# Kernel optimization log

Hardware: AMD Instinct MI355X
Metric: run time of the kernel (lower is better)

The kernel has to match this reference:

```python
import jax, jax.numpy as jnp
import numpy as np

P_BU = 0.5  # y_bottom_up_percent
P_TD = 1.0 - P_BU
EPS = 1e-12


def l2n(w):
    # F.normalize(w, dim=1)
    n = jnp.linalg.norm(w, axis=1, keepdims=True)
    return w / jnp.maximum(n, EPS)


def setup_inputs() -> dict:
    key = jax.random.key(0)
    ks = jax.random.split(key, 5)
    X, Y, Z = 64 * 64, 16384, 100
    return {
        "x": jax.random.normal(ks[0], (1, 64, 64), dtype=jnp.float32),
        "z": jax.random.randint(ks[1], (1,), 0, Z, dtype=jnp.int64 if jax.config.jax_enable_x64 else jnp.int32).astype(jnp.int32),
        "per_item": 10,
        "x2y_w": jax.random.uniform(ks[2], (Y, X), dtype=jnp.float32),
        "z2y_w": jax.random.uniform(ks[3], (Y, Z), dtype=jnp.float32),
        "y2z_w": jax.random.uniform(ks[4], (Z, Y), dtype=jnp.float32),
        "age_y": jnp.zeros((Y,), dtype=jnp.float32),
        "age_z": jnp.zeros((Z,), dtype=jnp.float32),
        "thr": jnp.zeros((Y,), dtype=jnp.float32),
    }


def _train_loop(xv, zh, z_idx, per_item, x2y_w, z2y_w, y2z_w, age_y, age_z, thr):
    Y = age_y.shape[0]

    def step(carry, _):
        x2y_w, z2y_w, y2z_w, age_y, age_z, thr = carry
        x2y_w = l2n(x2y_w)
        z2y_w = l2n(z2y_w)
        y2z_w = l2n(y2z_w)
        # pre-response: bottom-up + top-down, shape [Y]
        y_pre = (P_BU * (xv @ x2y_w.T) + P_TD * (zh @ z2y_w.T))[0]
        i0 = jnp.argmax(y_pre)
        r0 = y_pre[i0]
        # top_k_competition(flag=1): keep winner if above threshold or young
        keep = (r0 > thr[i0]) | (age_y[i0] < 1.0)
        unact = jnp.where(age_y >= 1.0, 0.0, 1.0)
        has_unact = jnp.sum(unact) > 0
        alt = jnp.argmax(y_pre * unact)
        win = jnp.where(keep, i0, jnp.where(has_unact, alt, i0))
        # Hebbian/EMA row updates with lr = 1/(age+1) (age before increment)
        lr = 1.0 / (age_y[win] + 1.0)
        x2y_w = x2y_w.at[win].set((1.0 - lr) * x2y_w[win] + lr * xv[0])
        z2y_w = z2y_w.at[win].set((1.0 - lr) * z2y_w[win] + lr * zh[0])
        age_y = age_y.at[win].add(1.0)
        zlr = (1.0 / (age_z[z_idx] + 1.0)) * zh[0, z_idx]
        y_onehot = jnp.zeros((Y,), x2y_w.dtype).at[win].set(1.0)
        y2z_w = y2z_w.at[z_idx].set((1.0 - zlr) * y2z_w[z_idx] + zlr * y_onehot)
        age_z = age_z.at[z_idx].add(1.0)
        thr = thr.at[win].set(lr * r0 + (1.0 - lr) * thr[win])
        return (x2y_w, z2y_w, y2z_w, age_y, age_z, thr), None

    carry, _ = jax.lax.scan(step, (x2y_w, z2y_w, y2z_w, age_y, age_z, thr), None, length=per_item)
    return carry


def reference(x, z, per_item, x2y_w, z2y_w, y2z_w, age_y, age_z, thr):
    # mode == 'train' path of DN.forward, batch = 1
    xv = x.reshape(1, -1)
    xv = xv / jnp.maximum(jnp.linalg.norm(xv, axis=1, keepdims=True), EPS)
    Z = z2y_w.shape[1]
    zh = jax.nn.one_hot(z, Z, dtype=xv.dtype)  # one-hot is already unit L2 norm
    z_idx = z[0]

    x2y_w, z2y_w, y2z_w, age_y, age_z, thr = _train_loop(
        xv, zh, z_idx, per_item, x2y_w, z2y_w, y2z_w, age_y, age_z, thr)

    x2y_w = l2n(x2y_w)
    y2z_w = l2n(y2z_w)
    y_flag = jnp.where(age_y >= 1.0, 1.0, 0.0)  # activated-neuron mask
    y_temp = (xv @ x2y_w.T) * y_flag[None, :]
    # top_k_competition(flag=0): one-hot at argmax
    y = jnp.zeros_like(y_temp).at[0, jnp.argmax(y_temp[0])].set(1.0)
    output = y @ y2z_w.T  # trans_y forward is identity on y_act
    y_activated_num = jnp.sum(y_flag)
    return output, y_activated_num
```

## Files before the change

kernel.cpp:

```cpp
#include <hip/hip_runtime.h>
#include <cmath>

#define EPSN 1e-12f
#define CHUNK 128
#define NCH 128
#define NTL 128
#define MAPCAP 16

__device__ __forceinline__ void amax_combine(float& v, int& i, float ov, int oi) {
    if (ov > v || (ov == v && oi < i)) { v = ov; i = oi; }
}
__device__ __forceinline__ void wave_amax(float& v, int& i) {
    for (int off = 32; off; off >>= 1) {
        float a = __shfl_down(v, off, 64);
        int b = __shfl_down(i, off, 64);
        amax_combine(v, i, a, b);
    }
}

__global__ __launch_bounds__(256) void k_prep(
    const float* __restrict__ x2y, const float* __restrict__ z2y,
    const float* __restrict__ y2z, const int* __restrict__ zptr,
    const float* __restrict__ x,
    float* __restrict__ dotx, float* __restrict__ nw2,
    float* __restrict__ valz, float* __restrict__ nz2,
    float* __restrict__ nry, float* __restrict__ xn2, int* __restrict__ cnti,
    int X, int Y, int Z)
{
    const int bid = blockIdx.x;
    const int NBZ = Y / 4;
    const int tid = threadIdx.x;
    const int lane = tid & 63, wv = tid >> 6;
    if (bid < NBZ) {
        const int zv = zptr[0];
        const int row = bid * 4 + wv;
        const float* r = z2y + (size_t)row * Z;
        float q = 0.f, v = 0.f;
        for (int j = lane; j < Z; j += 64) {
            float e = r[j];
            q += e * e;
            if (j == zv) v = e;
        }
        for (int off = 32; off; off >>= 1) {
            q += __shfl_down(q, off, 64);
            v += __shfl_down(v, off, 64);
        }
        if (lane == 0) { nz2[row] = q; valz[row] = v; }
    } else if (bid < NBZ + Z) {
        const int row = bid - NBZ;
        const float4* r4 = (const float4*)(y2z + (size_t)row * Y);
        float q = 0.f;
        for (int i = tid; i < (Y >> 2); i += 256) {
            float4 w = r4[i];
            q += w.x*w.x + w.y*w.y + w.z*w.z + w.w*w.w;
        }
        for (int off = 32; off; off >>= 1) q += __shfl_down(q, off, 64);
        __shared__ float sq[4];
        if (lane == 0) sq[wv] = q;
        __syncthreads();
        if (tid == 0) nry[row] = sq[0] + sq[1] + sq[2] + sq[3];
    } else if (bid < NBZ + Z + Y) {
        const int row = bid - NBZ - Z;
        const float4* w4 = (const float4*)(x2y + (size_t)row * X);
        const float4* x4 = (const float4*)x;
        float d = 0.f, q = 0.f;
        for (int i = tid; i < (X >> 2); i += 256) {
            float4 w = w4[i]; float4 xx = x4[i];
            d += w.x*xx.x + w.y*xx.y + w.z*xx.z + w.w*xx.w;
            q += w.x*w.x + w.y*w.y + w.z*w.z + w.w*w.w;
        }
        for (int off = 32; off; off >>= 1) {
            d += __shfl_down(d, off, 64);
            q += __shfl_down(q, off, 64);
        }
        __shared__ float sd[4], sq2[4];
        if (lane == 0) { sd[wv] = d; sq2[wv] = q; }
        __syncthreads();
        if (tid == 0) {
            dotx[row] = sd[0] + sd[1] + sd[2] + sd[3];
            nw2[row]  = sq2[0] + sq2[1] + sq2[2] + sq2[3];
        }
    } else {
        const float4* x4 = (const float4*)x;
        float q = 0.f;
        for (int i = tid; i < (X >> 2); i += 256) {
            float4 xx = x4[i];
            q += xx.x*xx.x + xx.y*xx.y + xx.z*xx.z + xx.w*xx.w;
        }
        for (int off = 32; off; off >>= 1) q += __shfl_down(q, off, 64);
        __shared__ float sq3[4];
        if (lane == 0) sq3[wv] = q;
        __syncthreads();
        if (tid == 0) { xn2[0] = sq3[0]+sq3[1]+sq3[2]+sq3[3]; cnti[0] = 0; }
    }
}

__global__ __launch_bounds__(NTL) void k_combine(
    const float* __restrict__ age_y_in, const float* __restrict__ thr_in,
    const float* __restrict__ y2z, const int* __restrict__ zptr,
    const float* __restrict__ dotx, const float* __restrict__ nw2,
    const float* __restrict__ valz, const float* __restrict__ nz2,
    const float* __restrict__ xn2,
    float* __restrict__ yp_ws, float* __restrict__ cA_ws,
    float* __restrict__ chv, int* __restrict__ chi,
    float* __restrict__ chcv, int* __restrict__ chci,
    float* __restrict__ cthr, float* __restrict__ cage,
    float* __restrict__ cvz, float* __restrict__ cnz,
    float* __restrict__ cyz, float* __restrict__ ccc,
    int* __restrict__ cnti, int Y)
{
    const int b = blockIdx.x, t = threadIdx.x;
    const int e = b * CHUNK + t;
    const int lane = t & 63, wv = t >> 6;
    const int zv = zptr[0];
    const float xn = fmaxf(sqrtf(xn2[0]), EPSN);
    const float vz_e = valz[e], nz_e = nz2[e];
    const float thr_e = thr_in[e];
    const float yz_e = y2z[(size_t)zv * Y + e];
    const float c = dotx[e] / (fmaxf(sqrtf(nw2[e]), EPSN) * xn);
    const float s = vz_e / fmaxf(sqrtf(nz_e), EPSN);
    const float ypv = 0.5f * (c + s);
    const float agev = age_y_in[e];
    const int young = agev < 1.0f;
    cA_ws[e] = c;
    yp_ws[e] = ypv;
    float v1 = ypv; int i1 = e;
    float v2 = c * (young ? 0.0f : 1.0f); int i2 = e;
    int yc = young;
    wave_amax(v1, i1);
    wave_amax(v2, i2);
    for (int off = 32; off; off >>= 1) yc += __shfl_down(yc, off, 64);
    __shared__ float s1v[2]; __shared__ int s1i[2];
    __shared__ float s2v[2]; __shared__ int s2i[2];
    __shared__ int syc[2]; __shared__ int sh_c1;
    if (lane == 0) { s1v[wv] = v1; s1i[wv] = i1; s2v[wv] = v2; s2i[wv] = i2; syc[wv] = yc; }
    __syncthreads();
    if (t == 0) {
        float a = s1v[0]; int ai = s1i[0];
        amax_combine(a, ai, s1v[1], s1i[1]);
        float bmv = s2v[0]; int bmi = s2i[0];
        amax_combine(bmv, bmi, s2v[1], s2i[1]);
        chv[b] = a; chi[b] = ai; chcv[b] = bmv; chci[b] = bmi;
        sh_c1 = ai;
        atomicAdd(cnti, syc[0] + syc[1]);
    }
    __syncthreads();
    if (e == sh_c1) {
        cthr[b] = thr_e; cage[b] = agev; cvz[b] = vz_e;
        cnz[b] = nz_e;   cyz[b] = yz_e;  ccc[b] = c;
    }
}

#define UPD(WIN, Gthr, Gage, Gvz, Gnz, Gy2z, Gc) do { \
    const int w_ = (WIN); \
    float age_o = (Gage), thr_o = (Gthr), c_o = (Gc); \
    float s_o = (Gvz) / fmaxf(sqrtf((Gnz)), EPSN); \
    int e_ = -1; \
    _Pragma("unroll") \
    for (int k_ = 0; k_ < MAPCAP; ++k_) if (wmI[k_] == w_) { \
        age_o = wmAge[k_]; thr_o = wmThr[k_]; s_o = wmS[k_]; c_o = wmC[k_]; e_ = k_; } \
    const float lr_ = 1.f/(age_o+1.f), om_ = 1.f-lr_; \
    const float cn_ = (om_*c_o+lr_)/fmaxf(sqrtf(om_*om_+lr_*lr_+2.f*lr_*om_*c_o), EPSN); \
    const float sn_ = (om_*s_o+lr_)/fmaxf(sqrtf(om_*om_+lr_*lr_+2.f*lr_*om_*s_o), EPSN); \
    if (e_ < 0) { e_ = wmn; wmn++; } \
    _Pragma("unroll") \
    for (int k_ = 0; k_ < MAPCAP; ++k_) if (k_ == e_) { \
        wmI[k_] = w_; wmAge[k_] = age_o + 1.f; wmThr[k_] = lr_*r0 + om_*thr_o; \
        wmS[k_] = sn_; wmC[k_] = cn_; wmYp[k_] = 0.5f*(cn_+sn_); } \
    if (age_o < 1.f && age_o + 1.f >= 1.f) cnt--; \
    { const int cw_ = (w_) >> 7; \
      if (lane == (cw_ & 63)) { \
        if (cw_ & 64) amax_combine(chc1, chcI1, cn_, w_); \
        else          amax_combine(chc0, chcI0, cn_, w_); } } \
    const float L_ = fmaxf(sqrtf(beta*beta*N0sq + 2.f*beta*Aacc + Bacc), EPSN); \
    beta /= L_; Aacc /= L_; Bacc /= (L_*L_); \
    _Pragma("unroll") \
    for (int k_ = 0; k_ < MAPCAP; ++k_) ymG[k_] /= L_; \
    const float zlr_ = 1.f/(agez+1.f), oz_ = 1.f-zlr_; \
    beta *= oz_; Aacc *= oz_; Bacc *= oz_*oz_; \
    _Pragma("unroll") \
    for (int k_ = 0; k_ < MAPCAP; ++k_) ymG[k_] *= oz_; \
    int q_ = -1; \
    _Pragma("unroll") \
    for (int k_ = 0; k_ < MAPCAP; ++k_) if (ymI[k_] == w_) q_ = k_; \
    if (q_ < 0) { q_ = ymn; ymn++; \
        _Pragma("unroll") \
        for (int k_ = 0; k_ < MAPCAP; ++k_) if (k_ == q_) { \
            ymI[k_] = w_; ymG[k_] = 0.f; ymV0[k_] = (Gy2z); } } \
    float gold_ = 0.f, v0_ = 0.f; \
    _Pragma("unroll") \
    for (int k_ = 0; k_ < MAPCAP; ++k_) if (k_ == q_) { gold_ = ymG[k_]; v0_ = ymV0[k_]; } \
    Bacc += 2.f*zlr_*gold_ + zlr_*zlr_; \
    Aacc += zlr_*v0_; \
    _Pragma("unroll") \
    for (int k_ = 0; k_ < MAPCAP; ++k_) if (k_ == q_) ymG[k_] = gold_ + zlr_; \
    agez += 1.f; \
    win = w_; \
} while (0)

__global__ __launch_bounds__(64) void k_loop(
    const int* __restrict__ zptr, const int* __restrict__ pitem,
    const float* __restrict__ y2z,
    const float* __restrict__ age_y_in, const float* __restrict__ age_z_in,
    const float* __restrict__ thr_in,
    const float* __restrict__ valz, const float* __restrict__ nz2,
    const float* __restrict__ nry,
    const float* __restrict__ yp_ws, const float* __restrict__ cA_ws,
    const float* __restrict__ chv_g, const int* __restrict__ chi_g,
    const float* __restrict__ chcv_g, const int* __restrict__ chci_g,
    const float* __restrict__ cthr, const float* __restrict__ cage,
    const float* __restrict__ cvz, const float* __restrict__ cnz,
    const float* __restrict__ cyz, const float* __restrict__ ccc,
    const int* __restrict__ cnti,
    float* __restrict__ out, int Y, int Z)
{
    const int lane = threadIdx.x;
    const int zv = zptr[0];
    const float* __restrict__ y2zrow = y2z + (size_t)zv * Y;

    float chv0 = chv_g[lane], chv1 = chv_g[lane + 64];
    int   chi0 = chi_g[lane], chi1 = chi_g[lane + 64];
    float chc0 = chcv_g[lane], chc1 = chcv_g[lane + 64];
    int   chcI0 = chci_g[lane], chcI1 = chci_g[lane + 64];
    float pthr0 = cthr[lane], pthr1 = cthr[lane + 64];
    float page0 = cage[lane], page1 = cage[lane + 64];
    float pvz0  = cvz[lane],  pvz1  = cvz[lane + 64];
    float pnz0  = cnz[lane],  pnz1  = cnz[lane + 64];
    float pyz0  = cyz[lane],  pyz1  = cyz[lane + 64];
    float pca0  = ccc[lane],  pca1  = ccc[lane + 64];

    int cnt = cnti[0];
    float N0sq = nry[zv], agez = age_z_in[zv];
    float beta = 1.f, Aacc = 0.f, Bacc = 0.f;
    int wmn = 0, ymn = 0;
    int   wmI[MAPCAP]; float wmAge[MAPCAP], wmThr[MAPCAP], wmS[MAPCAP], wmC[MAPCAP], wmYp[MAPCAP];
    int   ymI[MAPCAP]; float ymG[MAPCAP], ymV0[MAPCAP];
#pragma unroll
    for (int k = 0; k < MAPCAP; ++k) {
        wmI[k] = -1; wmAge[k] = 0.f; wmThr[k] = 0.f; wmS[k] = 0.f; wmC[k] = 0.f; wmYp[k] = 0.f;
        ymI[k] = -1; ymG[k] = 0.f; ymV0[k] = 0.f;
    }

    const int PI = pitem[0];
    for (int t = 0; t < PI; ++t) {
        float v = chv0; int i = chi0;
        amax_combine(v, i, chv1, chi1);
        wave_amax(v, i);
        const float r0 = __shfl(v, 0);
        const int   i0 = __shfl(i, 0);
        const int ts = i0 >> 7;
        const int sl = ts & 63;
        const bool hi = (ts & 64) != 0;
        const float bthr = __shfl(hi ? pthr1 : pthr0, sl);
        const float bage = __shfl(hi ? page1 : page0, sl);
        const float bvz  = __shfl(hi ? pvz1  : pvz0,  sl);
        const float bnz  = __shfl(hi ? pnz1  : pnz0,  sl);
        const float byz  = __shfl(hi ? pyz1  : pyz0,  sl);
        const float bca  = __shfl(hi ? pca1  : pca0,  sl);
        float age0 = bage, thr0 = bthr;
#pragma unroll
        for (int k = 0; k < MAPCAP; ++k)
            if (wmI[k] == i0) { age0 = wmAge[k]; thr0 = wmThr[k]; }
        const bool keep = (r0 > thr0) || (age0 < 1.f);
        int win;
        if (keep) {
            UPD(i0, bthr, bage, bvz, bnz, byz, bca);
        } else {
            float mv = -INFINITY; int mi = 0;
            for (int e = lane; e < Y; e += 64) {
                float vv = yp_ws[e];
                float ag = age_y_in[e];
#pragma unroll
                for (int k = 0; k < MAPCAP; ++k)
                    if (wmI[k] == e) { vv = wmYp[k]; ag = wmAge[k]; }
                const float m = vv * (ag < 1.f ? 1.f : 0.f);
                amax_combine(mv, mi, m, e);
            }
            wave_amax(mv, mi);
            const int alt = __shfl(mi, 0);
            if (cnt > 0) {
                const float gthr = thr_in[alt], gage = age_y_in[alt];
                const float gvz = valz[alt],   gnz = nz2[alt];
                const float gy  = y2zrow[alt], gc = cA_ws[alt];
                UPD(alt, gthr, gage, gvz, gnz, gy, gc);
            } else {
                UPD(i0, bthr, bage, bvz, bnz, byz, bca);
            }
        }
        const int cw = win >> 7;
        const int base = cw * CHUNK;
        float vA = yp_ws[base + lane];
        float vB = yp_ws[base + 64 + lane];
        int iA = base + lane, iB = base + 64 + lane;
#pragma unroll
        for (int k = 0; k < MAPCAP; ++k) {
            if (wmI[k] == iA) vA = wmYp[k];
            if (wmI[k] == iB) vB = wmYp[k];
        }
        amax_combine(vA, iA, vB, iB);
        wave_amax(vA, iA);
        const float nv = __shfl(vA, 0);
        const int   ni = __shfl(iA, 0);
        const float nthr = thr_in[ni], nage = age_y_in[ni];
        const float nvz = valz[ni],   nnz = nz2[ni];
        const float nyz = y2zrow[ni], nca = cA_ws[ni];
        if (lane == (cw & 63)) {
            if (cw & 64) {
                chv1 = nv; chi1 = ni;
                pthr1 = nthr; page1 = nage; pvz1 = nvz; pnz1 = nnz; pyz1 = nyz; pca1 = nca;
            } else {
                chv0 = nv; chi0 = ni;
                pthr0 = nthr; page0 = nage; pvz0 = nvz; pnz0 = nnz; pyz0 = nyz; pca0 = nca;
            }
        }
    }

    float fv = chc0; int fi = chcI0;
    amax_combine(fv, fi, chc1, chcI1);
    wave_amax(fv, fi);
    const int winf = __shfl(fi, 0);
    const float actn = (float)Y - (float)cnt;
    const float L = fmaxf(sqrtf(beta*beta*N0sq + 2.f*beta*Aacc + Bacc), EPSN);
    float g = 0.f, v0wf = y2zrow[winf];
#pragma unroll
    for (int k = 0; k < MAPCAP; ++k)
        if (ymI[k] == winf) { g = ymG[k]; v0wf = ymV0[k]; }
    const float outz = (beta * v0wf + g) / L;
    for (int e = lane; e < Z; e += 64) {
        const float o = (e == zv) ? outz
            : y2z[(size_t)e * Y + winf] / fmaxf(sqrtf(nry[e]), EPSN);
        out[e] = o;
    }
    if (lane == 0) out[Z] = actn;
}

extern "C" void kernel_launch(void* const* d_in, const int* in_sizes, int n_in,
                              void* d_out, int out_size, void* d_ws, size_t ws_size,
                              hipStream_t stream) {
    const float* x    = (const float*)d_in[0];
    const int*   z    = (const int*)d_in[1];
    const int*   pit  = (const int*)d_in[2];
    const float* x2y  = (const float*)d_in[3];
    const float* z2y  = (const float*)d_in[4];
    const float* y2z  = (const float*)d_in[5];
    const float* agey = (const float*)d_in[6];
    const float* agez = (const float*)d_in[7];
    const float* thr  = (const float*)d_in[8];
    const int X = in_sizes[0];
    const int Y = in_sizes[6];
    const int Z = in_sizes[7];

    float* ws = (float*)d_ws;
    float* dotx = ws;
    float* nw2  = ws + (size_t)Y;
    float* valz = ws + 2*(size_t)Y;
    float* nz2  = ws + 3*(size_t)Y;
    float* nry  = ws + 4*(size_t)Y;
    float* xn2  = ws + 4*(size_t)Y + 128;
    int*   cnti = (int*)(ws + 4*(size_t)Y + 129);
    float* ypw  = ws + 4*(size_t)Y + 256;
    float* cAw  = ws + 5*(size_t)Y + 256;
    float* base6 = ws + 6*(size_t)Y + 256;
    float* chv  = base6;
    int*   chi  = (int*)(base6 + NCH);
    float* chcv = base6 + 2*NCH;
    int*   chci = (int*)(base6 + 3*NCH);
    float* cthr = base6 + 4*NCH;
    float* cage = base6 + 5*NCH;
    float* cvz  = base6 + 6*NCH;
    float* cnz  = base6 + 7*NCH;
    float* cyz  = base6 + 8*NCH;
    float* ccc  = base6 + 9*NCH;
    float* out  = (float*)d_out;

    const int NBZ = Y / 4;
    const int grid_prep = NBZ + Z + Y + 1;
    hipLaunchKernelGGL(k_prep, dim3(grid_prep), dim3(256), 0, stream,
                       x2y, z2y, y2z, z, x, dotx, nw2, valz, nz2, nry, xn2, cnti, X, Y, Z);
    hipLaunchKernelGGL(k_combine, dim3(Y / CHUNK), dim3(NTL), 0, stream,
                       agey, thr, y2z, z, dotx, nw2, valz, nz2, xn2,
                       ypw, cAw, chv, chi, chcv, chci,
                       cthr, cage, cvz, cnz, cyz, ccc, cnti, Y);
    hipLaunchKernelGGL(k_loop, dim3(1), dim3(64), 0, stream,
                       z, pit, y2z, agey, agez, thr, valz, nz2, nry,
                       ypw, cAw, chv, chi, chcv, chci,
                       cthr, cage, cvz, cnz, cyz, ccc, cnti, out, Y, Z);
}
```

Before: 88.34 us.

## Replace register-resident update maps with live global arrays and wave-distributed y-map

The sequential loop kernel used to track per-winner updates in 16-entry register arrays that were scanned linearly on every lookup. It now writes the updated age, threshold, cosine terms and response straight into live global arrays filled by the combine kernel. The y2z row map is spread one entry per lane and searched with ballot and shuffle. This cuts register pressure and the unrolled scans on the serial critical path, at the cost of extra global writes in k_combine and dependent global loads inside the single-wave loop.

Result: faster. 75.27 us (median of 2 runs) (-14.8%).

```diff
diff --git a/kernel.cpp b/kernel.cpp
--- a/kernel.cpp
+++ b/kernel.cpp
@@ -5,7 +5,6 @@
 #define CHUNK 128
 #define NCH 128
 #define NTL 128
-#define MAPCAP 16
 
 __device__ __forceinline__ void amax_combine(float& v, int& i, float ov, int oi) {
     if (ov > v || (ov == v && oi < i)) { v = ov; i = oi; }
@@ -97,33 +96,30 @@
 
 __global__ __launch_bounds__(NTL) void k_combine(
     const float* __restrict__ age_y_in, const float* __restrict__ thr_in,
-    const float* __restrict__ y2z, const int* __restrict__ zptr,
     const float* __restrict__ dotx, const float* __restrict__ nw2,
     const float* __restrict__ valz, const float* __restrict__ nz2,
     const float* __restrict__ xn2,
-    float* __restrict__ yp_ws, float* __restrict__ cA_ws,
+    float* __restrict__ yp_live, float* __restrict__ cA_live,
+    float* __restrict__ s_live, float* __restrict__ age_live,
+    float* __restrict__ thr_live,
     float* __restrict__ chv, int* __restrict__ chi,
     float* __restrict__ chcv, int* __restrict__ chci,
-    float* __restrict__ cthr, float* __restrict__ cage,
-    float* __restrict__ cvz, float* __restrict__ cnz,
-    float* __restrict__ cyz, float* __restrict__ ccc,
-    int* __restrict__ cnti, int Y)
+    int* __restrict__ cnti)
 {
     const int b = blockIdx.x, t = threadIdx.x;
     const int e = b * CHUNK + t;
     const int lane = t & 63, wv = t >> 6;
-    const int zv = zptr[0];
     const float xn = fmaxf(sqrtf(xn2[0]), EPSN);
-    const float vz_e = valz[e], nz_e = nz2[e];
-    const float thr_e = thr_in[e];
-    const float yz_e = y2z[(size_t)zv * Y + e];
     const float c = dotx[e] / (fmaxf(sqrtf(nw2[e]), EPSN) * xn);
-    const float s = vz_e / fmaxf(sqrtf(nz_e), EPSN);
+    const float s = valz[e] / fmaxf(sqrtf(nz2[e]), EPSN);
     const float ypv = 0.5f * (c + s);
     const float agev = age_y_in[e];
     const int young = agev < 1.0f;
-    cA_ws[e] = c;
-    yp_ws[e] = ypv;
+    cA_live[e] = c;
+    yp_live[e] = ypv;
+    s_live[e] = s;
+    age_live[e] = agev;
+    thr_live[e] = thr_in[e];
     float v1 = ypv; int i1 = e;
     float v2 = c * (young ? 0.0f : 1.0f); int i2 = e;
     int yc = young;
@@ -132,7 +128,7 @@
     for (int off = 32; off; off >>= 1) yc += __shfl_down(yc, off, 64);
     __shared__ float s1v[2]; __shared__ int s1i[2];
     __shared__ float s2v[2]; __shared__ int s2i[2];
-    __shared__ int syc[2]; __shared__ int sh_c1;
+    __shared__ int syc[2];
     if (lane == 0) { s1v[wv] = v1; s1i[wv] = i1; s2v[wv] = v2; s2i[wv] = i2; syc[wv] = yc; }
     __syncthreads();
     if (t == 0) {
@@ -141,76 +137,53 @@
         float bmv = s2v[0]; int bmi = s2i[0];
         amax_combine(bmv, bmi, s2v[1], s2i[1]);
         chv[b] = a; chi[b] = ai; chcv[b] = bmv; chci[b] = bmi;
-        sh_c1 = ai;
         atomicAdd(cnti, syc[0] + syc[1]);
     }
-    __syncthreads();
-    if (e == sh_c1) {
-        cthr[b] = thr_e; cage[b] = agev; cvz[b] = vz_e;
-        cnz[b] = nz_e;   cyz[b] = yz_e;  ccc[b] = c;
-    }
-}
-
-#define UPD(WIN, Gthr, Gage, Gvz, Gnz, Gy2z, Gc) do { \
-    const int w_ = (WIN); \
-    float age_o = (Gage), thr_o = (Gthr), c_o = (Gc); \
-    float s_o = (Gvz) / fmaxf(sqrtf((Gnz)), EPSN); \
-    int e_ = -1; \
-    _Pragma("unroll") \
-    for (int k_ = 0; k_ < MAPCAP; ++k_) if (wmI[k_] == w_) { \
-        age_o = wmAge[k_]; thr_o = wmThr[k_]; s_o = wmS[k_]; c_o = wmC[k_]; e_ = k_; } \
+}
+
+#define UPD(W, AGE, THR, CO, SO, Y0) do { \
+    const int w_ = (W); \
+    const float age_o = (AGE), thr_o = (THR), c_o = (CO), s_o = (SO); \
     const float lr_ = 1.f/(age_o+1.f), om_ = 1.f-lr_; \
     const float cn_ = (om_*c_o+lr_)/fmaxf(sqrtf(om_*om_+lr_*lr_+2.f*lr_*om_*c_o), EPSN); \
     const float sn_ = (om_*s_o+lr_)/fmaxf(sqrtf(om_*om_+lr_*lr_+2.f*lr_*om_*s_o), EPSN); \
-    if (e_ < 0) { e_ = wmn; wmn++; } \
-    _Pragma("unroll") \
-    for (int k_ = 0; k_ < MAPCAP; ++k_) if (k_ == e_) { \
-        wmI[k_] = w_; wmAge[k_] = age_o + 1.f; wmThr[k_] = lr_*r0 + om_*thr_o; \
-        wmS[k_] = sn_; wmC[k_] = cn_; wmYp[k_] = 0.5f*(cn_+sn_); } \
+    const float ypn_ = 0.5f*(cn_+sn_); \
+    yp_live[w_] = ypn_; cA_live[w_] = cn_; s_live[w_] = sn_; \
+    age_live[w_] = age_o + 1.f; thr_live[w_] = lr_*r0 + om_*thr_o; \
     if (age_o < 1.f && age_o + 1.f >= 1.f) cnt--; \
-    { const int cw_ = (w_) >> 7; \
+    { const int cw_ = w_ >> 7; \
       if (lane == (cw_ & 63)) { \
         if (cw_ & 64) amax_combine(chc1, chcI1, cn_, w_); \
         else          amax_combine(chc0, chcI0, cn_, w_); } } \
     const float L_ = fmaxf(sqrtf(beta*beta*N0sq + 2.f*beta*Aacc + Bacc), EPSN); \
-    beta /= L_; Aacc /= L_; Bacc /= (L_*L_); \
-    _Pragma("unroll") \
-    for (int k_ = 0; k_ < MAPCAP; ++k_) ymG[k_] /= L_; \
+    beta /= L_; Aacc /= L_; Bacc /= (L_*L_); ymG_l /= L_; \
     const float zlr_ = 1.f/(agez+1.f), oz_ = 1.f-zlr_; \
-    beta *= oz_; Aacc *= oz_; Bacc *= oz_*oz_; \
-    _Pragma("unroll") \
-    for (int k_ = 0; k_ < MAPCAP; ++k_) ymG[k_] *= oz_; \
-    int q_ = -1; \
-    _Pragma("unroll") \
-    for (int k_ = 0; k_ < MAPCAP; ++k_) if (ymI[k_] == w_) q_ = k_; \
-    if (q_ < 0) { q_ = ymn; ymn++; \
-        _Pragma("unroll") \
-        for (int k_ = 0; k_ < MAPCAP; ++k_) if (k_ == q_) { \
-            ymI[k_] = w_; ymG[k_] = 0.f; ymV0[k_] = (Gy2z); } } \
-    float gold_ = 0.f, v0_ = 0.f; \
-    _Pragma("unroll") \
-    for (int k_ = 0; k_ < MAPCAP; ++k_) if (k_ == q_) { gold_ = ymG[k_]; v0_ = ymV0[k_]; } \
+    beta *= oz_; Aacc *= oz_; Bacc *= oz_*oz_; ymG_l *= oz_; \
+    unsigned long long qm_ = __ballot(ymI_l == w_); \
+    int q_; \
+    if (qm_ == 0ull) { \
+        q_ = ymn; \
+        if (lane == q_) { ymI_l = w_; ymG_l = 0.f; ymV0_l = (Y0); } \
+        ymn++; \
+    } else q_ = (int)__ffsll((long long)qm_) - 1; \
+    const float gold_ = __shfl(ymG_l, q_); \
+    const float v0_   = __shfl(ymV0_l, q_); \
     Bacc += 2.f*zlr_*gold_ + zlr_*zlr_; \
     Aacc += zlr_*v0_; \
-    _Pragma("unroll") \
-    for (int k_ = 0; k_ < MAPCAP; ++k_) if (k_ == q_) ymG[k_] = gold_ + zlr_; \
+    if (lane == q_) ymG_l = gold_ + zlr_; \
     agez += 1.f; \
-    win = w_; \
+    win = w_; ypnew = ypn_; \
 } while (0)
 
 __global__ __launch_bounds__(64) void k_loop(
     const int* __restrict__ zptr, const int* __restrict__ pitem,
     const float* __restrict__ y2z,
-    const float* __restrict__ age_y_in, const float* __restrict__ age_z_in,
-    const float* __restrict__ thr_in,
-    const float* __restrict__ valz, const float* __restrict__ nz2,
-    const float* __restrict__ nry,
-    const float* __restrict__ yp_ws, const float* __restrict__ cA_ws,
+    const float* __restrict__ age_z_in, const float* __restrict__ nry,
+    float* __restrict__ yp_live, float* __restrict__ cA_live,
+    float* __restrict__ s_live, float* __restrict__ age_live,
+    float* __restrict__ thr_live,
     const float* __restrict__ chv_g, const int* __restrict__ chi_g,
     const float* __restrict__ chcv_g, const int* __restrict__ chci_g,
-    const float* __restrict__ cthr, const float* __restrict__ cage,
-    const float* __restrict__ cvz, const float* __restrict__ cnz,
-    const float* __restrict__ cyz, const float* __restrict__ ccc,
     const int* __restrict__ cnti,
     float* __restrict__ out, int Y, int Z)
 {
@@ -222,24 +195,12 @@
     int   chi0 = chi_g[lane], chi1 = chi_g[lane + 64];
     float chc0 = chcv_g[lane], chc1 = chcv_g[lane + 64];
     int   chcI0 = chci_g[lane], chcI1 = chci_g[lane + 64];
-    float pthr0 = cthr[lane], pthr1 = cthr[lane + 64];
-    float page0 = cage[lane], page1 = cage[lane + 64];
-    float pvz0  = cvz[lane],  pvz1  = cvz[lane + 64];
-    float pnz0  = cnz[lane],  pnz1  = cnz[lane + 64];
-    float pyz0  = cyz[lane],  pyz1  = cyz[lane + 64];
-    float pca0  = ccc[lane],  pca1  = ccc[lane + 64];
 
     int cnt = cnti[0];
     float N0sq = nry[zv], agez = age_z_in[zv];
     float beta = 1.f, Aacc = 0.f, Bacc = 0.f;
-    int wmn = 0, ymn = 0;
-    int   wmI[MAPCAP]; float wmAge[MAPCAP], wmThr[MAPCAP], wmS[MAPCAP], wmC[MAPCAP], wmYp[MAPCAP];
-    int   ymI[MAPCAP]; float ymG[MAPCAP], ymV0[MAPCAP];
-#pragma unroll
-    for (int k = 0; k < MAPCAP; ++k) {
-        wmI[k] = -1; wmAge[k] = 0.f; wmThr[k] = 0.f; wmS[k] = 0.f; wmC[k] = 0.f; wmYp[k] = 0.f;
-        ymI[k] = -1; ymG[k] = 0.f; ymV0[k] = 0.f;
-    }
+    int ymn = 0;
+    int ymI_l = -1; float ymG_l = 0.f, ymV0_l = 0.f;
 
     const int PI = pitem[0];
     for (int t = 0; t < PI; ++t) {
@@ -248,70 +209,52 @@
         wave_amax(v, i);
         const float r0 = __shfl(v, 0);
         const int   i0 = __shfl(i, 0);
-        const int ts = i0 >> 7;
-        const int sl = ts & 63;
-        const bool hi = (ts & 64) != 0;
-        const float bthr = __shfl(hi ? pthr1 : pthr0, sl);
-        const float bage = __shfl(hi ? page1 : page0, sl);
-        const float bvz  = __shfl(hi ? pvz1  : pvz0,  sl);
-        const float bnz  = __shfl(hi ? pnz1  : pnz0,  sl);
-        const float byz  = __shfl(hi ? pyz1  : pyz0,  sl);
-        const float bca  = __shfl(hi ? pca1  : pca0,  sl);
-        float age0 = bage, thr0 = bthr;
-#pragma unroll
-        for (int k = 0; k < MAPCAP; ++k)
-            if (wmI[k] == i0) { age0 = wmAge[k]; thr0 = wmThr[k]; }
-        const bool keep = (r0 > thr0) || (age0 < 1.f);
-        int win;
+        const float a_i0 = age_live[i0];
+        const float t_i0 = thr_live[i0];
+        const float c_i0 = cA_live[i0];
+        const float s_i0 = s_live[i0];
+        const float y_i0 = y2zrow[i0];
+        const int base0 = (i0 >> 7) * CHUNK;
+        const float rA = yp_live[base0 + lane];
+        const float rB = yp_live[base0 + 64 + lane];
+        const bool keep = (r0 > t_i0) || (a_i0 < 1.f);
+        int win; float ypnew;
         if (keep) {
-            UPD(i0, bthr, bage, bvz, bnz, byz, bca);
+            UPD(i0, a_i0, t_i0, c_i0, s_i0, y_i0);
         } else {
             float mv = -INFINITY; int mi = 0;
             for (int e = lane; e < Y; e += 64) {
-                float vv = yp_ws[e];
-                float ag = age_y_in[e];
-#pragma unroll
-                for (int k = 0; k < MAPCAP; ++k)
-                    if (wmI[k] == e) { vv = wmYp[k]; ag = wmAge[k]; }
+                const float vv = yp_live[e];
+                const float ag = age_live[e];
                 const float m = vv * (ag < 1.f ? 1.f : 0.f);
                 amax_combine(mv, mi, m, e);
             }
             wave_amax(mv, mi);
             const int alt = __shfl(mi, 0);
             if (cnt > 0) {
-                const float gthr = thr_in[alt], gage = age_y_in[alt];
-                const float gvz = valz[alt],   gnz = nz2[alt];
-                const float gy  = y2zrow[alt], gc = cA_ws[alt];
-                UPD(alt, gthr, gage, gvz, gnz, gy, gc);
+                const float a_a = age_live[alt], t_a = thr_live[alt];
+                const float c_a = cA_live[alt],  s_a = s_live[alt];
+                const float y_a = y2zrow[alt];
+                UPD(alt, a_a, t_a, c_a, s_a, y_a);
             } else {
-                UPD(i0, bthr, bage, bvz, bnz, byz, bca);
+                UPD(i0, a_i0, t_i0, c_i0, s_i0, y_i0);
             }
         }
         const int cw = win >> 7;
         const int base = cw * CHUNK;
-        float vA = yp_ws[base + lane];
-        float vB = yp_ws[base + 64 + lane];
+        float vA, vB;
+        if (base == base0) { vA = rA; vB = rB; }
+        else { vA = yp_live[base + lane]; vB = yp_live[base + 64 + lane]; }
         int iA = base + lane, iB = base + 64 + lane;
-#pragma unroll
-        for (int k = 0; k < MAPCAP; ++k) {
-            if (wmI[k] == iA) vA = wmYp[k];
-            if (wmI[k] == iB) vB = wmYp[k];
-        }
+        if (iA == win) vA = ypnew;
+        if (iB == win) vB = ypnew;
         amax_combine(vA, iA, vB, iB);
         wave_amax(vA, iA);
         const float nv = __shfl(vA, 0);
         const int   ni = __shfl(iA, 0);
-        const float nthr = thr_in[ni], nage = age_y_in[ni];
-        const float nvz = valz[ni],   nnz = nz2[ni];
-        const float nyz = y2zrow[ni], nca = cA_ws[ni];
         if (lane == (cw & 63)) {
-            if (cw & 64) {
-                chv1 = nv; chi1 = ni;
-                pthr1 = nthr; page1 = nage; pvz1 = nvz; pnz1 = nnz; pyz1 = nyz; pca1 = nca;
-            } else {
-                chv0 = nv; chi0 = ni;
-                pthr0 = nthr; page0 = nage; pvz0 = nvz; pnz0 = nnz; pyz0 = nyz; pca0 = nca;
-            }
+            if (cw & 64) { chv1 = nv; chi1 = ni; }
+            else         { chv0 = nv; chi0 = ni; }
         }
     }
 
@@ -321,10 +264,15 @@
     const int winf = __shfl(fi, 0);
     const float actn = (float)Y - (float)cnt;
     const float L = fmaxf(sqrtf(beta*beta*N0sq + 2.f*beta*Aacc + Bacc), EPSN);
-    float g = 0.f, v0wf = y2zrow[winf];
-#pragma unroll
-    for (int k = 0; k < MAPCAP; ++k)
-        if (ymI[k] == winf) { g = ymG[k]; v0wf = ymV0[k]; }
+    float g = 0.f, v0wf;
+    const unsigned long long fm = __ballot(ymI_l == winf);
+    if (fm != 0ull) {
+        const int k = (int)__ffsll((long long)fm) - 1;
+        g = __shfl(ymG_l, k);
+        v0wf = __shfl(ymV0_l, k);
+    } else {
+        v0wf = y2zrow[winf];
+    }
     const float outz = (beta * v0wf + g) / L;
     for (int e = lane; e < Z; e += 64) {
         const float o = (e == zv) ? outz
@@ -358,19 +306,16 @@
     float* nry  = ws + 4*(size_t)Y;
     float* xn2  = ws + 4*(size_t)Y + 128;
     int*   cnti = (int*)(ws + 4*(size_t)Y + 129);
-    float* ypw  = ws + 4*(size_t)Y + 256;
-    float* cAw  = ws + 5*(size_t)Y + 256;
-    float* base6 = ws + 6*(size_t)Y + 256;
-    float* chv  = base6;
-    int*   chi  = (int*)(base6 + NCH);
-    float* chcv = base6 + 2*NCH;
-    int*   chci = (int*)(base6 + 3*NCH);
-    float* cthr = base6 + 4*NCH;
-    float* cage = base6 + 5*NCH;
-    float* cvz  = base6 + 6*NCH;
-    float* cnz  = base6 + 7*NCH;
-    float* cyz  = base6 + 8*NCH;
-    float* ccc  = base6 + 9*NCH;
+    float* ypl  = ws + 4*(size_t)Y + 256;
+    float* cAl  = ws + 5*(size_t)Y + 256;
+    float* sl   = ws + 6*(size_t)Y + 256;
+    float* agl  = ws + 7*(size_t)Y + 256;
+    float* thl  = ws + 8*(size_t)Y + 256;
+    float* base9 = ws + 9*(size_t)Y + 256;
+    float* chv  = base9;
+    int*   chi  = (int*)(base9 + NCH);
+    float* chcv = base9 + 2*NCH;
+    int*   chci = (int*)(base9 + 3*NCH);
     float* out  = (float*)d_out;
 
     const int NBZ = Y / 4;
@@ -378,11 +323,10 @@
     hipLaunchKernelGGL(k_prep, dim3(grid_prep), dim3(256), 0, stream,
                        x2y, z2y, y2z, z, x, dotx, nw2, valz, nz2, nry, xn2, cnti, X, Y, Z);
     hipLaunchKernelGGL(k_combine, dim3(Y / CHUNK), dim3(NTL), 0, stream,
-                       agey, thr, y2z, z, dotx, nw2, valz, nz2, xn2,
-                       ypw, cAw, chv, chi, chcv, chci,
-                       cthr, cage, cvz, cnz, cyz, ccc, cnti, Y);
+                       agey, thr, dotx, nw2, valz, nz2, xn2,
+                       ypl, cAl, sl, agl, thl, chv, chi, chcv, chci, cnti);
     hipLaunchKernelGGL(k_loop, dim3(1), dim3(64), 0, stream,
-                       z, pit, y2z, agey, agez, thr, valz, nz2, nry,
-                       ypw, cAw, chv, chi, chcv, chci,
-                       cthr, cage, cvz, cnz, cyz, ccc, cnti, out, Y, Z);
-}
+                       z, pit, y2z, agez, nry,
+                       ypl, cAl, sl, agl, thl,
+                       chv, chi, chcv, chci, cnti, out, Y, Z);
+}
```
